# Kernel optimization log

Measured on AMD Instinct MI355X. Metric: run time of the kernel, lower is better.

The kernel has to match this reference:

```python
import jax, jax.numpy as jnp
import numpy as np


def setup_inputs() -> dict:
    key = jax.random.key(0)
    k1, k2 = jax.random.split(key)
    B, C, H, W = 2, 512, 128, 256
    refimg_fea = jax.random.normal(k1, (B, C, H, W), dtype=jnp.float32)
    targetimg_fea = jax.random.normal(k2, (B, C, H, W), dtype=jnp.float32)
    return {
        "refimg_fea": refimg_fea,
        "targetimg_fea": targetimg_fea,
        "num_groups": 8,
        "maxdisp": 48,
    }


def reference(refimg_fea, targetimg_fea, num_groups, maxdisp):
    # Group-wise correlation cost volume.
    # Torch version: left-pad target by (maxdisp-1), unfold width-maxdisp windows,
    # multiply with ref, sum over per-group channels, then flip the disparity axis.
    # Equivalent direct form: volume[b,g,d,h,w] = sum_c ref[b,g,c,h,w] * tgt[b,g,c,h,w-d]
    # (zero where w-d < 0), for d in [0, maxdisp).
    B, C, H, W = refimg_fea.shape
    G = num_groups
    Cg = C // G
    ref = refimg_fea.reshape(B, G, Cg, H, W)
    tgt = targetimg_fea.reshape(B, G, Cg, H, W)
    # zero-pad target on the left of the width axis
    padded = jnp.pad(tgt, ((0, 0), (0, 0), (0, 0), (0, 0), (maxdisp - 1, 0)))
    slices = []
    for d in range(maxdisp):  # small fixed loop over disparities (static slices)
        start = maxdisp - 1 - d
        tgt_d = padded[..., start:start + W]  # target shifted right by d
        slices.append(jnp.einsum('bgchw,bgchw->bghw', ref, tgt_d))
    volume = jnp.stack(slices, axis=2)  # [B, G, maxdisp, H, W]
    return volume
```

## Files before the change

kernel.cpp:

```cpp
#include <hip/hip_runtime.h>

#define NBG 16
#define HH 128
#define WW 256
#define CGR 64
#define ND 48
#define TPB 256
#define PITCH 40
#define OPITCH 132

typedef __attribute__((ext_vector_type(8))) short short8v;
typedef __attribute__((ext_vector_type(4))) float float4v;

__device__ __forceinline__ short f2bf(float x) {
    unsigned u = __builtin_bit_cast(unsigned, x);
    u += 0x7fffu + ((u >> 16) & 1u);
    return (short)(u >> 16);
}

union SMem {
    struct {
        short refT[128][PITCH];
        short tgtT[176][PITCH];
    } s;
    float outb[ND][OPITCH];
};

__global__ __launch_bounds__(TPB, 6)
void gwc_mfma(const float* __restrict__ ref, const float* __restrict__ tgt,
              float* __restrict__ out) {
    __shared__ __align__(16) SMem sm;

    const int tid  = threadIdx.x;
    const int lane = tid & 63;
    const int wv   = tid >> 6;
    const int fr   = lane & 15;
    const int fhi  = lane >> 4;

    const int blk  = blockIdx.x;
    const int half = blk & 1;
    const int h    = (blk >> 1) & (HH - 1);
    const int bg   = blk >> 8;
    const int W0   = half * 128;

    const size_t cstride = (size_t)HH * WW;
    const float* refbase = ref + ((size_t)bg * CGR * HH + h) * WW;
    const float* tgtbase = tgt + ((size_t)bg * CGR * HH + h) * WW;

    float4v acc[2][4];
    #pragma unroll
    for (int j = 0; j < 2; ++j)
        #pragma unroll
        for (int i = 0; i < 4; ++i)
            acc[j][i] = (float4v){0.f, 0.f, 0.f, 0.f};

    for (int ch = 0; ch < 2; ++ch) {
        if (ch) __syncthreads();
        const int c0 = ch * 32;
        #pragma unroll
        for (int rr = 0; rr < 2; ++rr) {
            const int row = tid + rr * 256;
            if (row < 304) {
                const bool isref = row < 128;
                const int  r  = isref ? row : row - 128;
                const int  wg = isref ? (W0 + r) : (W0 - 48 + r);
                short* dst = isref ? &sm.s.refT[r][0] : &sm.s.tgtT[r][0];
                if (wg >= 0) {
                    const float* p = (isref ? refbase : tgtbase) + (size_t)c0 * cstride + wg;
                    float v[32];
                    #pragma unroll
                    for (int cc = 0; cc < 32; ++cc) v[cc] = p[(size_t)cc * cstride];
                    #pragma unroll
                    for (int gq = 0; gq < 8; ++gq)
                        *(short4*)(dst + 4 * gq) =
                            make_short4(f2bf(v[4*gq]), f2bf(v[4*gq+1]),
                                        f2bf(v[4*gq+2]), f2bf(v[4*gq+3]));
                } else {
                    #pragma unroll
                    for (int gq = 0; gq < 8; ++gq)
                        *(short4*)(dst + 4 * gq) = make_short4(0, 0, 0, 0);
                }
            }
        }
        __syncthreads();
        const short8v bfr0 = *(const short8v*)&sm.s.refT[16 * wv + fr][8 * fhi];
        const short8v bfr1 = *(const short8v*)&sm.s.refT[16 * (wv + 4) + fr][8 * fhi];
        #pragma unroll
        for (int j = 0; j < 2; ++j) {
            #pragma unroll
            for (int i = 0; i < 4; ++i) {
                const int mt = wv + 4 * j + i;
                const short8v afr = *(const short8v*)&sm.s.tgtT[16 * mt + fr][8 * fhi];
                acc[j][i] = __builtin_amdgcn_mfma_f32_16x16x32_bf16(
                    afr, (j ? bfr1 : bfr0), acc[j][i], 0, 0, 0);
            }
        }
    }

    __syncthreads();
    #pragma unroll
    for (int j = 0; j < 2; ++j) {
        const int wl = 16 * (wv + 4 * j) + fr;
        #pragma unroll
        for (int i = 0; i < 4; ++i)
            #pragma unroll
            for (int rg = 0; rg < 4; ++rg) {
                const int d = 48 - 16 * i + fr - 4 * fhi - rg;
                if ((unsigned)d < (unsigned)ND)
                    sm.outb[d][wl] = acc[j][i][rg];
            }
    }
    __syncthreads();
    for (int s = tid; s < ND * 32; s += TPB) {
        const int dd = s >> 5;
        const int wq = s & 31;
        const float4 v = *(const float4*)&sm.outb[dd][4 * wq];
        *(float4*)(out + ((size_t)(bg * ND + dd) * HH + h) * WW + W0 + 4 * wq) = v;
    }
}

extern "C" void kernel_launch(void* const* d_in, const int* in_sizes, int n_in,
                              void* d_out, int out_size, void* d_ws, size_t ws_size,
                              hipStream_t stream) {
    const float* ref = (const float*)d_in[0];
    const float* tgt = (const float*)d_in[1];
    float* out = (float*)d_out;
    const int grid = NBG * HH * 2;
    gwc_mfma<<<dim3(grid), dim3(TPB), 0, stream>>>(ref, tgt, out);
}
```

Baseline: 76.24 us.

## Load all 64 channels in one pass with 512 threads and swizzled block order

Switches to 512 threads per block. Each block stages all 64 channels of ref and target into one shared-memory tile in a single pass, with each thread loading 16-channel chunks for up to three rows, instead of two sequential 32-channel passes separated by a barrier. Each wave then does two MFMAs per tile, one per half of the K dimension. Blocks are remapped so that consecutive launched blocks are spread across batch-groups. The aim is to expose more memory parallelism and drop a sync phase, at the cost of larger shared memory and more registers, with fewer blocks resident per CU.

Result: slower. 81.56 us (+7.0%).

```diff
diff --git a/kernel.cpp b/kernel.cpp
--- a/kernel.cpp
+++ b/kernel.cpp
@@ -1,12 +1,11 @@
 #include <hip/hip_runtime.h>
 
-#define NBG 16
 #define HH 128
 #define WW 256
 #define CGR 64
 #define ND 48
-#define TPB 256
-#define PITCH 40
+#define TPB 512
+#define PITCH 72
 #define OPITCH 132
 
 typedef __attribute__((ext_vector_type(8))) short short8v;
@@ -19,14 +18,11 @@
 }
 
 union SMem {
-    struct {
-        short refT[128][PITCH];
-        short tgtT[176][PITCH];
-    } s;
+    short st[304][PITCH];
     float outb[ND][OPITCH];
 };
 
-__global__ __launch_bounds__(TPB, 6)
+__global__ __launch_bounds__(TPB, 4)
 void gwc_mfma(const float* __restrict__ ref, const float* __restrict__ tgt,
               float* __restrict__ out) {
     __shared__ __align__(16) SMem sm;
@@ -37,85 +33,88 @@
     const int fr   = lane & 15;
     const int fhi  = lane >> 4;
 
-    const int blk  = blockIdx.x;
+    const int blk  = ((blockIdx.x & 7) << 9) | (blockIdx.x >> 3);
     const int half = blk & 1;
     const int h    = (blk >> 1) & (HH - 1);
     const int bg   = blk >> 8;
-    const int W0   = half * 128;
+    const int W0   = half << 7;
 
     const size_t cstride = (size_t)HH * WW;
     const float* refbase = ref + ((size_t)bg * CGR * HH + h) * WW;
     const float* tgtbase = tgt + ((size_t)bg * CGR * HH + h) * WW;
 
-    float4v acc[2][4];
+    float v0[16], v1[16], v2[16];
+    int q0, r0, q1, r1, q2, r2; bool ok0, ok1, ok2;
+    {
+        const int j0 = tid;        q0 = j0 / 320; r0 = j0 % 320; ok0 = r0 < 304;
+        const int j1 = tid + 512;  q1 = j1 / 320; r1 = j1 % 320; ok1 = r1 < 304;
+        const int j2 = tid + 1024; q2 = j2 / 320; r2 = j2 % 320; ok2 = (tid < 256) && (r2 < 304);
+    }
+#define ISSUE(V, OK, Q, R)                                                        \
+    if (OK) {                                                                     \
+        const int wg = (R < 128) ? (W0 + R) : (W0 - 176 + R);                     \
+        const float* p = ((R < 128) ? refbase : tgtbase) +                        \
+                         (size_t)(Q * 16) * cstride + wg;                         \
+        const bool ld = wg >= 0;                                                  \
+        _Pragma("unroll")                                                         \
+        for (int cc = 0; cc < 16; ++cc) V[cc] = ld ? p[(size_t)cc * cstride] : 0.0f; \
+    }
+    ISSUE(v0, ok0, q0, r0)
+    ISSUE(v1, ok1, q1, r1)
+    ISSUE(v2, ok2, q2, r2)
+#undef ISSUE
+
+#define CONVERT(V, OK, Q, R)                                                      \
+    if (OK) {                                                                     \
+        short* dst = &sm.st[R][16 * Q];                                           \
+        _Pragma("unroll")                                                         \
+        for (int g = 0; g < 4; ++g)                                               \
+            *(short4*)(dst + 4 * g) = make_short4(f2bf(V[4*g]), f2bf(V[4*g+1]),   \
+                                                  f2bf(V[4*g+2]), f2bf(V[4*g+3]));\
+    }
+    CONVERT(v0, ok0, q0, r0)
+    CONVERT(v1, ok1, q1, r1)
+    CONVERT(v2, ok2, q2, r2)
+#undef CONVERT
+
+    __syncthreads();
+
+    float4v acc[4];
     #pragma unroll
-    for (int j = 0; j < 2; ++j)
-        #pragma unroll
-        for (int i = 0; i < 4; ++i)
-            acc[j][i] = (float4v){0.f, 0.f, 0.f, 0.f};
+    for (int i = 0; i < 4; ++i) acc[i] = (float4v){0.f, 0.f, 0.f, 0.f};
 
-    for (int ch = 0; ch < 2; ++ch) {
-        if (ch) __syncthreads();
-        const int c0 = ch * 32;
-        #pragma unroll
-        for (int rr = 0; rr < 2; ++rr) {
-            const int row = tid + rr * 256;
-            if (row < 304) {
-                const bool isref = row < 128;
-                const int  r  = isref ? row : row - 128;
-                const int  wg = isref ? (W0 + r) : (W0 - 48 + r);
-                short* dst = isref ? &sm.s.refT[r][0] : &sm.s.tgtT[r][0];
-                if (wg >= 0) {
-                    const float* p = (isref ? refbase : tgtbase) + (size_t)c0 * cstride + wg;
-                    float v[32];
-                    #pragma unroll
-                    for (int cc = 0; cc < 32; ++cc) v[cc] = p[(size_t)cc * cstride];
-                    #pragma unroll
-                    for (int gq = 0; gq < 8; ++gq)
-                        *(short4*)(dst + 4 * gq) =
-                            make_short4(f2bf(v[4*gq]), f2bf(v[4*gq+1]),
-                                        f2bf(v[4*gq+2]), f2bf(v[4*gq+3]));
-                } else {
-                    #pragma unroll
-                    for (int gq = 0; gq < 8; ++gq)
-                        *(short4*)(dst + 4 * gq) = make_short4(0, 0, 0, 0);
-                }
-            }
-        }
-        __syncthreads();
-        const short8v bfr0 = *(const short8v*)&sm.s.refT[16 * wv + fr][8 * fhi];
-        const short8v bfr1 = *(const short8v*)&sm.s.refT[16 * (wv + 4) + fr][8 * fhi];
-        #pragma unroll
-        for (int j = 0; j < 2; ++j) {
-            #pragma unroll
-            for (int i = 0; i < 4; ++i) {
-                const int mt = wv + 4 * j + i;
-                const short8v afr = *(const short8v*)&sm.s.tgtT[16 * mt + fr][8 * fhi];
-                acc[j][i] = __builtin_amdgcn_mfma_f32_16x16x32_bf16(
-                    afr, (j ? bfr1 : bfr0), acc[j][i], 0, 0, 0);
-            }
-        }
+    const short* brow = &sm.st[16 * wv + fr][8 * fhi];
+    const short8v bfr0 = *(const short8v*)brow;
+    const short8v bfr1 = *(const short8v*)(brow + 32);
+    #pragma unroll
+    for (int i = 0; i < 4; ++i) {
+        const int mt = wv + i;
+        const short* arow = &sm.st[128 + 16 * mt + fr][8 * fhi];
+        acc[i] = __builtin_amdgcn_mfma_f32_16x16x32_bf16(
+                     *(const short8v*)arow, bfr0, acc[i], 0, 0, 0);
+        acc[i] = __builtin_amdgcn_mfma_f32_16x16x32_bf16(
+                     *(const short8v*)(arow + 32), bfr1, acc[i], 0, 0, 0);
     }
 
     __syncthreads();
+
+    const int wl = 16 * wv + fr;
     #pragma unroll
-    for (int j = 0; j < 2; ++j) {
-        const int wl = 16 * (wv + 4 * j) + fr;
+    for (int i = 0; i < 4; ++i)
         #pragma unroll
-        for (int i = 0; i < 4; ++i)
-            #pragma unroll
-            for (int rg = 0; rg < 4; ++rg) {
-                const int d = 48 - 16 * i + fr - 4 * fhi - rg;
-                if ((unsigned)d < (unsigned)ND)
-                    sm.outb[d][wl] = acc[j][i][rg];
-            }
-    }
+        for (int rg = 0; rg < 4; ++rg) {
+            const int d = 48 - 16 * i + fr - 4 * fhi - rg;
+            if ((unsigned)d < (unsigned)ND) sm.outb[d][wl] = acc[i][rg];
+        }
     __syncthreads();
-    for (int s = tid; s < ND * 32; s += TPB) {
-        const int dd = s >> 5;
-        const int wq = s & 31;
-        const float4 v = *(const float4*)&sm.outb[dd][4 * wq];
-        *(float4*)(out + ((size_t)(bg * ND + dd) * HH + h) * WW + W0 + 4 * wq) = v;
+
+    #pragma unroll
+    for (int k = 0; k < 3; ++k) {
+        const int idx = tid + 512 * k;
+        const int dd  = idx >> 5;
+        const int wq  = idx & 31;
+        const float4 vv = *(const float4*)&sm.outb[dd][4 * wq];
+        *(float4*)(out + ((size_t)(bg * ND + dd) * HH + h) * WW + W0 + 4 * wq) = vv;
     }
 }
 
@@ -125,6 +124,5 @@
     const float* ref = (const float*)d_in[0];
     const float* tgt = (const float*)d_in[1];
     float* out = (float*)d_out;
-    const int grid = NBG * HH * 2;
-    gwc_mfma<<<dim3(grid), dim3(TPB), 0, stream>>>(ref, tgt, out);
+    gwc_mfma<<<dim3(16 * HH * 2), dim3(TPB), 0, stream>>>(ref, tgt, out);
 }
```

## Load all 64 channels at once with coalesced float4 loads and transposed LDS writes

Applied to the files above, without the earlier changes.

The kernel now loads the whole 64-channel slab for ref and target in one phase. Each thread issues float4 loads that run along width, where before each thread walked 32 channels with scalar strided loads, and the two channel chunks needed separate synchronized passes. Values are converted to bf16 and scattered transposed into a single LDS array with an odd-ish pitch of 66, and fragments are read back with 4 dword loads. Block indices are remapped so the 8 consecutive blocks belong to different group and batch slices, and the occupancy hint drops from 6 to 4 to allow 19 float4 registers in flight. Possible costs are more LDS bank conflicts from the scalar transposed short writes, fragment loads that are no longer a single 128-bit read, and lower occupancy.

Result: slower. 79.98 us (+4.9%).

```diff
diff --git a/kernel.cpp b/kernel.cpp
--- a/kernel.cpp
+++ b/kernel.cpp
@@ -1,12 +1,10 @@
 #include <hip/hip_runtime.h>
 
-#define NBG 16
 #define HH 128
 #define WW 256
-#define CGR 64
 #define ND 48
 #define TPB 256
-#define PITCH 40
+#define PITCH 66
 #define OPITCH 132
 
 typedef __attribute__((ext_vector_type(8))) short short8v;
@@ -18,15 +16,19 @@
     return (short)(u >> 16);
 }
 
+__device__ __forceinline__ short8v ld_frag(const short* p) {
+    union { int i[4]; short8v v; } u;
+    const int* q = (const int*)p;
+    u.i[0] = q[0]; u.i[1] = q[1]; u.i[2] = q[2]; u.i[3] = q[3];
+    return u.v;
+}
+
 union SMem {
-    struct {
-        short refT[128][PITCH];
-        short tgtT[176][PITCH];
-    } s;
+    short st[304 * PITCH];
     float outb[ND][OPITCH];
 };
 
-__global__ __launch_bounds__(TPB, 6)
+__global__ __launch_bounds__(TPB, 4)
 void gwc_mfma(const float* __restrict__ ref, const float* __restrict__ tgt,
               float* __restrict__ out) {
     __shared__ __align__(16) SMem sm;
@@ -37,85 +39,101 @@
     const int fr   = lane & 15;
     const int fhi  = lane >> 4;
 
-    const int blk  = blockIdx.x;
+    const int blk  = ((blockIdx.x & 7) << 9) | (blockIdx.x >> 3);
     const int half = blk & 1;
     const int h    = (blk >> 1) & (HH - 1);
     const int bg   = blk >> 8;
-    const int W0   = half * 128;
+    const int W0   = half << 7;
 
     const size_t cstride = (size_t)HH * WW;
-    const float* refbase = ref + ((size_t)bg * CGR * HH + h) * WW;
-    const float* tgtbase = tgt + ((size_t)bg * CGR * HH + h) * WW;
+    const float* refbase = ref + ((size_t)bg * 64 * HH + h) * WW;
+    const float* tgtbase = tgt + ((size_t)bg * 64 * HH + h) * WW;
+
+    float4 f[19];
+    {
+        const float* rp = refbase + (size_t)(tid >> 5) * cstride + (W0 + 4 * (tid & 31));
+        #pragma unroll
+        for (int p = 0; p < 8; ++p)
+            f[p] = *(const float4*)(rp + (size_t)(8 * p) * cstride);
+        #pragma unroll
+        for (int u = 0; u < 11; ++u) {
+            const int jt = tid + 256 * u;
+            const int cc = (int)((unsigned)jt / 44u);
+            const int q  = jt - 44 * cc;
+            const int wg = W0 - 48 + 4 * q;
+            const float* tp = tgtbase + (size_t)cc * cstride + (wg >= 0 ? wg : 0);
+            f[8 + u] = *(const float4*)tp;
+        }
+    }
+    __builtin_amdgcn_sched_barrier(0);
+    {
+        short* wp0 = &sm.st[(4 * (tid & 31)) * PITCH + (tid >> 5)];
+        #pragma unroll
+        for (int p = 0; p < 8; ++p) {
+            short* wp = wp0 + 8 * p;
+            wp[0 * PITCH] = f2bf(f[p].x);
+            wp[1 * PITCH] = f2bf(f[p].y);
+            wp[2 * PITCH] = f2bf(f[p].z);
+            wp[3 * PITCH] = f2bf(f[p].w);
+        }
+        #pragma unroll
+        for (int u = 0; u < 11; ++u) {
+            const int jt = tid + 256 * u;
+            const int cc = (int)((unsigned)jt / 44u);
+            const int q  = jt - 44 * cc;
+            const float vs = (W0 != 0 || q >= 12) ? 1.0f : 0.0f;
+            short* wp = &sm.st[(128 + 4 * q) * PITCH + cc];
+            wp[0 * PITCH] = f2bf(f[8 + u].x * vs);
+            wp[1 * PITCH] = f2bf(f[8 + u].y * vs);
+            wp[2 * PITCH] = f2bf(f[8 + u].z * vs);
+            wp[3 * PITCH] = f2bf(f[8 + u].w * vs);
+        }
+    }
+    __syncthreads();
 
     float4v acc[2][4];
     #pragma unroll
-    for (int j = 0; j < 2; ++j)
+    for (int t = 0; t < 2; ++t)
         #pragma unroll
-        for (int i = 0; i < 4; ++i)
-            acc[j][i] = (float4v){0.f, 0.f, 0.f, 0.f};
+        for (int i = 0; i < 4; ++i) acc[t][i] = (float4v){0.f, 0.f, 0.f, 0.f};
 
-    for (int ch = 0; ch < 2; ++ch) {
-        if (ch) __syncthreads();
-        const int c0 = ch * 32;
+    #pragma unroll
+    for (int s = 0; s < 2; ++s) {
+        const int ko = 8 * fhi + 32 * s;
         #pragma unroll
-        for (int rr = 0; rr < 2; ++rr) {
-            const int row = tid + rr * 256;
-            if (row < 304) {
-                const bool isref = row < 128;
-                const int  r  = isref ? row : row - 128;
-                const int  wg = isref ? (W0 + r) : (W0 - 48 + r);
-                short* dst = isref ? &sm.s.refT[r][0] : &sm.s.tgtT[r][0];
-                if (wg >= 0) {
-                    const float* p = (isref ? refbase : tgtbase) + (size_t)c0 * cstride + wg;
-                    float v[32];
-                    #pragma unroll
-                    for (int cc = 0; cc < 32; ++cc) v[cc] = p[(size_t)cc * cstride];
-                    #pragma unroll
-                    for (int gq = 0; gq < 8; ++gq)
-                        *(short4*)(dst + 4 * gq) =
-                            make_short4(f2bf(v[4*gq]), f2bf(v[4*gq+1]),
-                                        f2bf(v[4*gq+2]), f2bf(v[4*gq+3]));
-                } else {
-                    #pragma unroll
-                    for (int gq = 0; gq < 8; ++gq)
-                        *(short4*)(dst + 4 * gq) = make_short4(0, 0, 0, 0);
-                }
-            }
-        }
-        __syncthreads();
-        const short8v bfr0 = *(const short8v*)&sm.s.refT[16 * wv + fr][8 * fhi];
-        const short8v bfr1 = *(const short8v*)&sm.s.refT[16 * (wv + 4) + fr][8 * fhi];
-        #pragma unroll
-        for (int j = 0; j < 2; ++j) {
+        for (int t = 0; t < 2; ++t) {
+            const int nt = wv + 4 * t;
+            const short8v bf = ld_frag(&sm.st[(16 * nt + fr) * PITCH + ko]);
             #pragma unroll
             for (int i = 0; i < 4; ++i) {
-                const int mt = wv + 4 * j + i;
-                const short8v afr = *(const short8v*)&sm.s.tgtT[16 * mt + fr][8 * fhi];
-                acc[j][i] = __builtin_amdgcn_mfma_f32_16x16x32_bf16(
-                    afr, (j ? bfr1 : bfr0), acc[j][i], 0, 0, 0);
+                const short8v af = ld_frag(&sm.st[(128 + 16 * (nt + i) + fr) * PITCH + ko]);
+                acc[t][i] = __builtin_amdgcn_mfma_f32_16x16x32_bf16(af, bf, acc[t][i], 0, 0, 0);
             }
         }
     }
 
     __syncthreads();
+
     #pragma unroll
-    for (int j = 0; j < 2; ++j) {
-        const int wl = 16 * (wv + 4 * j) + fr;
+    for (int t = 0; t < 2; ++t) {
+        const int wl = 16 * (wv + 4 * t) + fr;
         #pragma unroll
         for (int i = 0; i < 4; ++i)
             #pragma unroll
             for (int rg = 0; rg < 4; ++rg) {
                 const int d = 48 - 16 * i + fr - 4 * fhi - rg;
-                if ((unsigned)d < (unsigned)ND)
-                    sm.outb[d][wl] = acc[j][i][rg];
+                if ((unsigned)d < (unsigned)ND) sm.outb[d][wl] = acc[t][i][rg];
             }
     }
     __syncthreads();
-    for (int s = tid; s < ND * 32; s += TPB) {
-        const int dd = s >> 5;
-        const int wq = s & 31;
-        const float4 v = *(const float4*)&sm.outb[dd][4 * wq];
-        *(float4*)(out + ((size_t)(bg * ND + dd) * HH + h) * WW + W0 + 4 * wq) = v;
+
+    #pragma unroll
+    for (int k = 0; k < 6; ++k) {
+        const int idx = tid + 256 * k;
+        const int dd  = idx >> 5;
+        const int wq  = idx & 31;
+        *(float4*)(out + ((size_t)(bg * ND + dd) * HH + h) * WW + W0 + 4 * wq) =
+            *(const float4*)&sm.outb[dd][4 * wq];
     }
 }
 
@@ -125,6 +143,5 @@
     const float* ref = (const float*)d_in[0];
     const float* tgt = (const float*)d_in[1];
     float* out = (float*)d_out;
-    const int grid = NBG * HH * 2;
-    gwc_mfma<<<dim3(grid), dim3(TPB), 0, stream>>>(ref, tgt, out);
+    gwc_mfma<<<dim3(16 * HH * 2), dim3(TPB), 0, stream>>>(ref, tgt, out);
 }
```
